# Optimization experiments

Hardware: AMD Instinct MI355X
Metric: run time of the kernel (lower is better)

## Reference

```python
import jax, jax.numpy as jnp
import numpy as np

N_ATOMS = 200
SEG_LEN = 1
N_FRAMES = 256


def _get_segments(n_atoms: int, length: int) -> np.ndarray:
    # All pairs of non-overlapping length-`length` segments [i, i+L, j, j+L], j - i > L.
    n_starts = n_atoms - length  # 199 segment start points
    i, j = np.triu_indices(n_starts, k=length + 1)
    return np.stack([i, i + length, j, j + length], axis=1).astype(np.int64)


def setup_inputs() -> dict:
    key = jax.random.key(0)
    xyz = jax.random.normal(key, (N_FRAMES, N_ATOMS, 3), dtype=jnp.float32) * 3.0
    segments = jnp.asarray(_get_segments(N_ATOMS, SEG_LEN))  # (19503, 4)
    return {"xyz": xyz, "segments": segments}


def _nnorm(x):
    return x / jnp.linalg.norm(x, axis=-1, keepdims=True)


def reference(xyz, segments):
    F = xyz.shape[0]
    S = segments.shape[0]
    # Gather the 4 endpoint coordinates per segment pair: (F, S, 4, 3)
    smat = xyz[:, segments]
    # displacements[a*2+b] = smat[2+b] - smat[a] for a,b in {0,1}: (F, S, 4, 3)
    disp = _nnorm((smat[:, :, None, 2:, :] - smat[:, :, :2, None, :]).reshape(F, S, 4, 3))
    idx_a = jnp.array([0, 1, 3, 2])
    idx_b = jnp.array([1, 3, 2, 0])
    crosses = _nnorm(jnp.cross(disp[:, :, idx_a], disp[:, :, idx_b]))  # (F, S, 4, 3)
    dots = jnp.sum(crosses * crosses[:, :, idx_b], axis=-1)  # (F, S, 4)
    omega = jnp.arcsin(jnp.clip(dots, -1.0, 1.0)).sum(-1)  # (F, S)
    signs = jnp.sign(
        jnp.sum(
            jnp.cross(smat[:, :, 3] - smat[:, :, 2], smat[:, :, 1] - smat[:, :, 0])
            * disp[:, :, 0],
            axis=-1,
        )
    )
    wr = (1.0 / (2.0 * jnp.pi)) * (omega * signs)
    return jnp.squeeze(wr)
```

## Files before the change

kernel.cpp:

```cpp
#include <hip/hip_runtime.h>
#include <math.h>

#define ATOMS 200

static __device__ __forceinline__ float3 f3(float x, float y, float z) {
    return make_float3(x, y, z);
}
static __device__ __forceinline__ float3 sub3(float3 a, float3 b) {
    return f3(a.x - b.x, a.y - b.y, a.z - b.z);
}
static __device__ __forceinline__ float dot3(float3 a, float3 b) {
    return fmaf(a.x, b.x, fmaf(a.y, b.y, a.z * b.z));
}
static __device__ __forceinline__ float3 cross3(float3 a, float3 b) {
    return f3(fmaf(a.y, b.z, -a.z * b.y),
              fmaf(a.z, b.x, -a.x * b.z),
              fmaf(a.x, b.y, -a.y * b.x));
}

static __device__ __forceinline__ float asin_fast(float x) {
    float a = fminf(fabsf(x), 1.0f);
    float t = __builtin_amdgcn_sqrtf(1.0f - a);
    float p = fmaf(a, -0.0187293f, 0.0742610f);
    p = fmaf(a, p, -0.2121144f);
    p = fmaf(a, p, 1.5707288f);
    float r = fmaf(-t, p, 1.5707963267948966f);
    return copysignf(r, x);
}

static __device__ __forceinline__ int row_base(int i, int m) {
    return i * m - (i * (i - 1)) / 2;
}

__global__ __launch_bounds__(256) void writhe_kernel(
    const float* __restrict__ xyz,
    float*       __restrict__ out,
    int S, int m )
{
    __shared__ float sx[ATOMS * 3];

    const int f = blockIdx.y;
    const float* fx = xyz + (size_t)f * (ATOMS * 3);
    for (int t = threadIdx.x; t < ATOMS * 3; t += blockDim.x)
        sx[t] = fx[t];
    __syncthreads();

    const int s = blockIdx.x * blockDim.x + threadIdx.x;
    if (s >= S) return;

    const float tm = 2.0f * (float)m + 1.0f;
    const float disc = fmaf(tm, tm, -8.0f * (float)s);
    int i = (int)(0.5f * (tm - __builtin_amdgcn_sqrtf(disc)));
    i = max(0, min(i, m - 1));
    while (i < m - 1 && row_base(i + 1, m) <= s) ++i;
    while (i > 0 && row_base(i, m) > s) --i;
    const int j = i + 2 + (s - row_base(i, m));

    const float3 p0 = f3(sx[3 * i],     sx[3 * i + 1], sx[3 * i + 2]);
    const float3 p1 = f3(sx[3 * i + 3], sx[3 * i + 4], sx[3 * i + 5]);
    const float3 p2 = f3(sx[3 * j],     sx[3 * j + 1], sx[3 * j + 2]);
    const float3 p3 = f3(sx[3 * j + 3], sx[3 * j + 4], sx[3 * j + 5]);

    const float3 e0 = sub3(p2, p0);
    const float3 e1 = sub3(p3, p0);
    const float3 e2 = sub3(p2, p1);
    const float3 e3 = sub3(p3, p1);

    const float3 u0 = cross3(e0, e1);
    const float3 u1 = cross3(e1, e3);
    const float3 u3 = cross3(e2, e0);

    const float n0 = dot3(u0, u0);
    const float n1 = dot3(u1, u1);
    const float n3 = dot3(u3, u3);

    const float d01 = dot3(u0, u1) * __builtin_amdgcn_rsqf(n0 * n1);
    const float d13 = dot3(u1, u3) * __builtin_amdgcn_rsqf(n1 * n3);
    const float d30 = dot3(u3, u0) * __builtin_amdgcn_rsqf(n3 * n0);

    const float half_pi = 1.5707963267948966f;
    const float omega = asin_fast(d01) + asin_fast(d13) + half_pi + asin_fast(d30);

    const float sv = -dot3(u0, e2);
    const float sgn = (sv > 0.0f) ? 1.0f : ((sv < 0.0f) ? -1.0f : 0.0f);

    const float inv2pi = 0.15915494309189535f;
    out[(size_t)f * S + s] = omega * sgn * inv2pi;
}

extern "C" void kernel_launch(void* const* d_in, const int* in_sizes, int n_in,
                              void* d_out, int out_size, void* d_ws, size_t ws_size,
                              hipStream_t stream)
{
    const float* xyz = (const float*)d_in[0];
    float*       out = (float*)d_out;

    const int F = in_sizes[0] / (ATOMS * 3);
    const int S = out_size / F;
    const int m = (int)((-1.0 + sqrt(1.0 + 8.0 * (double)S)) * 0.5 + 0.5);

    dim3 grid((S + 255) / 256, F);
    writhe_kernel<<<grid, 256, 0, stream>>>(xyz, out, S, m);
}
```

Measured before the change: 26.57 us.

## Compute four consecutive segment pairs per thread reusing shared cross products

Each thread now handles four consecutive pairs along a row, rolling the endpoint points and reusing the previous pair's displacement and cross product (u3 = -u1 prev), so fewer cross products and less index math run per output. The shared-memory staging and barrier are dropped in favour of direct global float3 loads. This amortises the triangular index inversion over four outputs, in exchange for fewer threads, uncoalesced per-thread strided stores, and unaligned 12-byte global loads.

```diff
diff --git a/kernel.cpp b/kernel.cpp
--- a/kernel.cpp
+++ b/kernel.cpp
@@ -2,6 +2,7 @@
 #include <math.h>
 
 #define ATOMS 200
+#define W 4
 
 static __device__ __forceinline__ float3 f3(float x, float y, float z) {
     return make_float3(x, y, z);
@@ -17,6 +18,9 @@
               fmaf(a.z, b.x, -a.x * b.z),
               fmaf(a.x, b.y, -a.y * b.x));
 }
+static __device__ __forceinline__ float3 neg3(float3 a) {
+    return f3(-a.x, -a.y, -a.z);
+}
 
 static __device__ __forceinline__ float asin_fast(float x) {
     float a = fminf(fabsf(x), 1.0f);
@@ -24,8 +28,7 @@
     float p = fmaf(a, -0.0187293f, 0.0742610f);
     p = fmaf(a, p, -0.2121144f);
     p = fmaf(a, p, 1.5707288f);
-    float r = fmaf(-t, p, 1.5707963267948966f);
-    return copysignf(r, x);
+    return copysignf(fmaf(-t, p, 1.5707963267948966f), x);
 }
 
 static __device__ __forceinline__ int row_base(int i, int m) {
@@ -37,55 +40,84 @@
     float*       __restrict__ out,
     int S, int m )
 {
-    __shared__ float sx[ATOMS * 3];
+    const int f = blockIdx.y;
+    const float3* __restrict__ P =
+        reinterpret_cast<const float3*>(xyz + (size_t)f * (ATOMS * 3));
 
-    const int f = blockIdx.y;
-    const float* fx = xyz + (size_t)f * (ATOMS * 3);
-    for (int t = threadIdx.x; t < ATOMS * 3; t += blockDim.x)
-        sx[t] = fx[t];
-    __syncthreads();
-
-    const int s = blockIdx.x * blockDim.x + threadIdx.x;
-    if (s >= S) return;
+    const int t = blockIdx.x * blockDim.x + threadIdx.x;
+    const int s0 = t * W;
+    if (s0 >= S) return;
 
     const float tm = 2.0f * (float)m + 1.0f;
-    const float disc = fmaf(tm, tm, -8.0f * (float)s);
+    const float disc = fmaf(tm, tm, -8.0f * (float)s0);
     int i = (int)(0.5f * (tm - __builtin_amdgcn_sqrtf(disc)));
     i = max(0, min(i, m - 1));
-    while (i < m - 1 && row_base(i + 1, m) <= s) ++i;
-    while (i > 0 && row_base(i, m) > s) --i;
-    const int j = i + 2 + (s - row_base(i, m));
+    while (i < m - 1 && row_base(i + 1, m) <= s0) ++i;
+    while (i > 0 && row_base(i, m) > s0) --i;
+    int j = i + 2 + (s0 - row_base(i, m));
+    const int jmax = m + 1;
 
-    const float3 p0 = f3(sx[3 * i],     sx[3 * i + 1], sx[3 * i + 2]);
-    const float3 p1 = f3(sx[3 * i + 3], sx[3 * i + 4], sx[3 * i + 5]);
-    const float3 p2 = f3(sx[3 * j],     sx[3 * j + 1], sx[3 * j + 2]);
-    const float3 p3 = f3(sx[3 * j + 3], sx[3 * j + 4], sx[3 * j + 5]);
+    const float3 q4 = P[min(j + 2, ATOMS - 1)];
+    const float3 q5 = P[min(j + 3, ATOMS - 1)];
+    const float3 q6 = P[min(j + 4, ATOMS - 1)];
 
-    const float3 e0 = sub3(p2, p0);
-    const float3 e1 = sub3(p3, p0);
-    const float3 e2 = sub3(p2, p1);
-    const float3 e3 = sub3(p3, p1);
+    float3 p0 = P[i], p1 = P[i + 1], p2 = P[j], p3 = P[j + 1];
+    float3 d0 = sub3(p2, p0), d2 = sub3(p2, p1);
+    float3 u1p = f3(0.f, 0.f, 0.f);
+    float  n1p = 0.f;
+    bool rolled = false, crossed = false;
 
-    const float3 u0 = cross3(e0, e1);
-    const float3 u1 = cross3(e1, e3);
-    const float3 u3 = cross3(e2, e0);
+    float res0 = 0.f, res1 = 0.f, res2 = 0.f, res3 = 0.f;
+    const float half_pi = 1.5707963267948966f;
+    const float inv2pi  = 0.15915494309189535f;
 
-    const float n0 = dot3(u0, u0);
-    const float n1 = dot3(u1, u1);
-    const float n3 = dot3(u3, u3);
+    #pragma unroll
+    for (int k = 0; k < W; ++k) {
+        const float3 d1 = sub3(p3, p0), d3 = sub3(p3, p1);
+        const float3 u0 = cross3(d0, d1);  const float n0 = dot3(u0, u0);
+        const float3 u1 = cross3(d1, d3);  const float n1 = dot3(u1, u1);
+        float3 u3; float n3;
+        if (rolled) { u3 = neg3(u1p);      n3 = n1p; }
+        else        { u3 = cross3(d2, d0); n3 = dot3(u3, u3); }
 
-    const float d01 = dot3(u0, u1) * __builtin_amdgcn_rsqf(n0 * n1);
-    const float d13 = dot3(u1, u3) * __builtin_amdgcn_rsqf(n1 * n3);
-    const float d30 = dot3(u3, u0) * __builtin_amdgcn_rsqf(n3 * n0);
+        const float d01 = dot3(u0, u1) * __builtin_amdgcn_rsqf(n0 * n1);
+        const float d13 = dot3(u1, u3) * __builtin_amdgcn_rsqf(n1 * n3);
+        const float d30 = dot3(u3, u0) * __builtin_amdgcn_rsqf(n3 * n0);
 
-    const float half_pi = 1.5707963267948966f;
-    const float omega = asin_fast(d01) + asin_fast(d13) + half_pi + asin_fast(d30);
+        const float omega =
+            asin_fast(d01) + asin_fast(d13) + half_pi + asin_fast(d30);
 
-    const float sv = -dot3(u0, e2);
-    const float sgn = (sv > 0.0f) ? 1.0f : ((sv < 0.0f) ? -1.0f : 0.0f);
+        const float sv  = -dot3(u0, d2);
+        const float sgn = (sv > 0.f) ? 1.f : ((sv < 0.f) ? -1.f : 0.f);
+        const float r   = omega * sgn * inv2pi;
+        if      (k == 0) res0 = r;
+        else if (k == 1) res1 = r;
+        else if (k == 2) res2 = r;
+        else             res3 = r;
 
-    const float inv2pi = 0.15915494309189535f;
-    out[(size_t)f * S + s] = omega * sgn * inv2pi;
+        if (k < W - 1 && s0 + k + 1 < S) {
+            ++j;
+            if (j > jmax) {
+                ++i; j = i + 2;
+                p0 = P[i]; p1 = P[i + 1]; p2 = P[j]; p3 = P[j + 1];
+                d0 = sub3(p2, p0); d2 = sub3(p2, p1);
+                rolled = false; crossed = true;
+            } else {
+                p2 = p3;
+                if (crossed) p3 = P[j + 1];
+                else         p3 = (k == 0) ? q4 : (k == 1) ? q5 : q6;
+                d0 = d1; d2 = d3;
+                u1p = u1; n1p = n1;
+                rolled = true;
+            }
+        }
+    }
+
+    float* o = out + (size_t)f * S + s0;
+    o[0] = res0;
+    if (s0 + 1 < S) o[1] = res1;
+    if (s0 + 2 < S) o[2] = res2;
+    if (s0 + 3 < S) o[3] = res3;
 }
 
 extern "C" void kernel_launch(void* const* d_in, const int* in_sizes, int n_in,
@@ -99,6 +131,7 @@
     const int S = out_size / F;
     const int m = (int)((-1.0 + sqrt(1.0 + 8.0 * (double)S)) * 0.5 + 0.5);
 
-    dim3 grid((S + 255) / 256, F);
+    const int s_threads = (S + W - 1) / W;
+    dim3 grid((s_threads + 255) / 256, F);
     writhe_kernel<<<grid, 256, 0, stream>>>(xyz, out, S, m);
 }
```

After: 25.62 us. 3.6% less time.

## Compute four consecutive j-segments per thread, reusing shared cross products

Applied to the files above, without the earlier changes.

Each thread now handles a chunk of up to four adjacent j positions in a row, so displacement vectors, one cross product and its norm carry over between neighbouring segment pairs instead of being recomputed. The shared-memory staging and barrier are dropped in favour of direct float3 global loads. Per-pair normalisation switches to separate rsq per cross product, reusing the carried one. This cuts thread count and arithmetic but gives unaligned, uncoalesced stores and loads and fewer waves.

```diff
diff --git a/kernel.cpp b/kernel.cpp
--- a/kernel.cpp
+++ b/kernel.cpp
@@ -2,6 +2,7 @@
 #include <math.h>
 
 #define ATOMS 200
+#define W 4
 
 static __device__ __forceinline__ float3 f3(float x, float y, float z) {
     return make_float3(x, y, z);
@@ -17,6 +18,9 @@
               fmaf(a.z, b.x, -a.x * b.z),
               fmaf(a.x, b.y, -a.y * b.x));
 }
+static __device__ __forceinline__ float3 neg3(float3 a) {
+    return f3(-a.x, -a.y, -a.z);
+}
 
 static __device__ __forceinline__ float asin_fast(float x) {
     float a = fminf(fabsf(x), 1.0f);
@@ -24,68 +28,102 @@
     float p = fmaf(a, -0.0187293f, 0.0742610f);
     p = fmaf(a, p, -0.2121144f);
     p = fmaf(a, p, 1.5707288f);
-    float r = fmaf(-t, p, 1.5707963267948966f);
-    return copysignf(r, x);
+    return copysignf(fmaf(-t, p, 1.5707963267948966f), x);
 }
 
-static __device__ __forceinline__ int row_base(int i, int m) {
-    return i * m - (i * (i - 1)) / 2;
+static __device__ __host__ __forceinline__ int C4(int K) {
+    int q = K >> 2, r = K & 3;
+    return 2 * q * (q + 1) + r * (q + 1);
+}
+
+struct St { float3 d1, d3, u1; float r1; };
+
+static __device__ __forceinline__ float wr_term(
+    float3 u0, float3 u1, float3 u3, float r0, float r1, float r3, float3 d2)
+{
+    const float d01 = dot3(u0, u1) * (r0 * r1);
+    const float d13 = dot3(u1, u3) * (r1 * r3);
+    const float d30 = dot3(u3, u0) * (r3 * r0);
+    const float omega = asin_fast(d01) + asin_fast(d13)
+                      + 1.5707963267948966f + asin_fast(d30);
+    const float sv  = -dot3(u0, d2);
+    const float sgn = (sv > 0.f) ? 1.f : ((sv < 0.f) ? -1.f : 0.f);
+    return omega * sgn * 0.15915494309189535f;
+}
+
+static __device__ __forceinline__ float elem_full(
+    float3 a0, float3 a1, float3 p2, float3 p3, St& st)
+{
+    const float3 d0 = sub3(p2, a0), d1 = sub3(p3, a0);
+    const float3 d2 = sub3(p2, a1), d3 = sub3(p3, a1);
+    const float3 u0 = cross3(d0, d1);
+    const float3 u1 = cross3(d1, d3);
+    const float3 u3 = cross3(d2, d0);
+    const float r0 = __builtin_amdgcn_rsqf(dot3(u0, u0));
+    const float r1 = __builtin_amdgcn_rsqf(dot3(u1, u1));
+    const float r3 = __builtin_amdgcn_rsqf(dot3(u3, u3));
+    st.d1 = d1; st.d3 = d3; st.u1 = u1; st.r1 = r1;
+    return wr_term(u0, u1, u3, r0, r1, r3, d2);
+}
+
+static __device__ __forceinline__ float elem_roll(
+    float3 a0, float3 a1, float3 p3, St& st)
+{
+    const float3 d0 = st.d1, d2 = st.d3;
+    const float3 d1 = sub3(p3, a0), d3 = sub3(p3, a1);
+    const float3 u0 = cross3(d0, d1);
+    const float3 u1 = cross3(d1, d3);
+    const float3 u3 = neg3(st.u1);
+    const float r0 = __builtin_amdgcn_rsqf(dot3(u0, u0));
+    const float r1 = __builtin_amdgcn_rsqf(dot3(u1, u1));
+    const float r3 = st.r1;
+    const float res = wr_term(u0, u1, u3, r0, r1, r3, d2);
+    st.d1 = d1; st.d3 = d3; st.u1 = u1; st.r1 = r1;
+    return res;
 }
 
 __global__ __launch_bounds__(256) void writhe_kernel(
     const float* __restrict__ xyz,
     float*       __restrict__ out,
-    int S, int m )
+    int S, int m , int CH )
 {
-    __shared__ float sx[ATOMS * 3];
+    const int f = blockIdx.y;
+    const float3* __restrict__ P =
+        reinterpret_cast<const float3*>(xyz + (size_t)f * (ATOMS * 3));
 
-    const int f = blockIdx.y;
-    const float* fx = xyz + (size_t)f * (ATOMS * 3);
-    for (int t = threadIdx.x; t < ATOMS * 3; t += blockDim.x)
-        sx[t] = fx[t];
-    __syncthreads();
+    const int g = blockIdx.x * blockDim.x + threadIdx.x;
+    if (g >= CH) return;
 
-    const int s = blockIdx.x * blockDim.x + threadIdx.x;
-    if (s >= S) return;
+    const int h = CH - g;
+    int K = (int)(__builtin_amdgcn_sqrtf(fmaf(8.f, (float)h, 4.f)) - 2.f);
+    K = max(1, min(K, m));
+    while (K < m && C4(K) < h) ++K;
+    while (K > 1 && C4(K - 1) >= h) --K;
 
-    const float tm = 2.0f * (float)m + 1.0f;
-    const float disc = fmaf(tm, tm, -8.0f * (float)s);
-    int i = (int)(0.5f * (tm - __builtin_amdgcn_sqrtf(disc)));
-    i = max(0, min(i, m - 1));
-    while (i < m - 1 && row_base(i + 1, m) <= s) ++i;
-    while (i > 0 && row_base(i, m) > s) --i;
-    const int j = i + 2 + (s - row_base(i, m));
+    const int i    = m - K;
+    const int c    = g - (CH - C4(K));
+    const int j0   = i + 2 + 4 * c;
+    const int nrem = min(W, K - 4 * c);
+    const int s0   = i * m - (i * (i - 1)) / 2 + 4 * c;
 
-    const float3 p0 = f3(sx[3 * i],     sx[3 * i + 1], sx[3 * i + 2]);
-    const float3 p1 = f3(sx[3 * i + 3], sx[3 * i + 4], sx[3 * i + 5]);
-    const float3 p2 = f3(sx[3 * j],     sx[3 * j + 1], sx[3 * j + 2]);
-    const float3 p3 = f3(sx[3 * j + 3], sx[3 * j + 4], sx[3 * j + 5]);
+    const float3 a0 = P[i], a1 = P[i + 1];
+    const float3 q0 = P[j0];
+    const float3 q1 = P[j0 + 1];
+    const float3 q2 = P[j0 + min(2, nrem)];
+    const float3 q3 = P[j0 + min(3, nrem)];
+    const float3 q4 = P[j0 + min(4, nrem)];
 
-    const float3 e0 = sub3(p2, p0);
-    const float3 e1 = sub3(p3, p0);
-    const float3 e2 = sub3(p2, p1);
-    const float3 e3 = sub3(p3, p1);
+    St st;
+    const float r0v = elem_full(a0, a1, q0, q1, st);
+    const float r1v = elem_roll(a0, a1, q2, st);
+    const float r2v = elem_roll(a0, a1, q3, st);
+    const float r3v = elem_roll(a0, a1, q4, st);
 
-    const float3 u0 = cross3(e0, e1);
-    const float3 u1 = cross3(e1, e3);
-    const float3 u3 = cross3(e2, e0);
-
-    const float n0 = dot3(u0, u0);
-    const float n1 = dot3(u1, u1);
-    const float n3 = dot3(u3, u3);
-
-    const float d01 = dot3(u0, u1) * __builtin_amdgcn_rsqf(n0 * n1);
-    const float d13 = dot3(u1, u3) * __builtin_amdgcn_rsqf(n1 * n3);
-    const float d30 = dot3(u3, u0) * __builtin_amdgcn_rsqf(n3 * n0);
-
-    const float half_pi = 1.5707963267948966f;
-    const float omega = asin_fast(d01) + asin_fast(d13) + half_pi + asin_fast(d30);
-
-    const float sv = -dot3(u0, e2);
-    const float sgn = (sv > 0.0f) ? 1.0f : ((sv < 0.0f) ? -1.0f : 0.0f);
-
-    const float inv2pi = 0.15915494309189535f;
-    out[(size_t)f * S + s] = omega * sgn * inv2pi;
+    float* o = out + (size_t)f * S + s0;
+    o[0] = r0v;
+    if (nrem > 1) o[1] = r1v;
+    if (nrem > 2) o[2] = r2v;
+    if (nrem > 3) o[3] = r3v;
 }
 
 extern "C" void kernel_launch(void* const* d_in, const int* in_sizes, int n_in,
@@ -99,6 +137,9 @@
     const int S = out_size / F;
     const int m = (int)((-1.0 + sqrt(1.0 + 8.0 * (double)S)) * 0.5 + 0.5);
 
-    dim3 grid((S + 255) / 256, F);
-    writhe_kernel<<<grid, 256, 0, stream>>>(xyz, out, S, m);
+    const int q = m >> 2, r = m & 3;
+    const int CH = 2 * q * (q + 1) + r * (q + 1);
+
+    dim3 grid((CH + 255) / 256, F);
+    writhe_kernel<<<grid, 256, 0, stream>>>(xyz, out, S, m, CH);
 }
```

New measurement: 22.69 us. 14.6% less time.
